# Performance work log

Measured on AMD Instinct MI355X. Metric: run time of the kernel, lower is better.

## Reference

```python
import jax, jax.numpy as jnp
import numpy as np
import math

B, H, S, DIM = 1, 16, 2048, 128

def _clin(xr, xi, wr, wi, br, bi):
    # complex linear: F.linear semantics -> x @ W.T
    out_r = xr @ wr.T - xi @ wi.T + br
    out_i = xr @ wi.T + xi @ wr.T + bi
    return out_r, out_i

def setup_inputs() -> dict:
    key = jax.random.key(0)
    ks = jax.random.split(key, 32)
    shp = (B, H, S, DIM)
    names = ["q_r", "q_i", "k_r", "k_i", "v_r", "v_i", "pe_q_r", "pe_q_i", "pe_k_r", "pe_k_i"]
    d = {n: jax.random.normal(ks[i], shp, jnp.float32) for i, n in enumerate(names)}
    wscale = 1.0 / math.sqrt(DIM)
    i = 10
    for p in ["q", "k", "v", "g", "o"]:
        d[p + "w_r"] = jax.random.normal(ks[i], (DIM, DIM), jnp.float32) * wscale; i += 1
        d[p + "w_i"] = jax.random.normal(ks[i], (DIM, DIM), jnp.float32) * wscale; i += 1
        d[p + "b_r"] = jnp.zeros((DIM,), jnp.float32)
        d[p + "b_i"] = jnp.zeros((DIM,), jnp.float32)
    return d

def reference(q_r, q_i, k_r, k_i, v_r, v_i, pe_q_r, pe_q_i, pe_k_r, pe_k_i,
              qw_r, qw_i, qb_r, qb_i, kw_r, kw_i, kb_r, kb_i,
              vw_r, vw_i, vb_r, vb_i, gw_r, gw_i, gb_r, gb_i,
              ow_r, ow_i, ob_r, ob_i):
    scale = DIM ** -0.5
    qr, qi = _clin(q_r, q_i, qw_r, qw_i, qb_r, qb_i)
    kr, ki = _clin(k_r, k_i, kw_r, kw_i, kb_r, kb_i)
    vr, vi = _clin(v_r, v_i, vw_r, vw_i, vb_r, vb_i)
    qr = qr + pe_q_r; qi = qi + pe_q_i
    kr = kr + pe_k_r; ki = ki + pe_k_i
    # complex QK^H -> real/imag parts, shapes [B,H,S,S]
    sr = jnp.einsum('bhqd,bhkd->bhqk', qr, kr) + jnp.einsum('bhqd,bhkd->bhqk', qi, ki)
    si = jnp.einsum('bhqd,bhkd->bhqk', qi, kr) - jnp.einsum('bhqd,bhkd->bhqk', qr, ki)
    scores = jnp.sqrt(sr * sr + si * si + 1e-8) * scale  # magnitude scores
    attn = jax.nn.softmax(scores, axis=-1)
    ar = attn @ vr
    ai = attn @ vi
    gr, gi = _clin(q_r, q_i, gw_r, gw_i, gb_r, gb_i)  # gate from raw q
    gar = gr * ar - gi * ai
    gai = gr * ai + gi * ar
    out_r, out_i = _clin(gar, gai, ow_r, ow_i, ob_r, ob_i)
    return (out_r, out_i, gr, gi)
```

## Files before the change

### kernel.cpp

```cpp
#include <hip/hip_runtime.h>
#include <math.h>

#define HH 16
#define SS 2048
#define DD 128
#define NROWS (HH * SS)
#define OUTSZ (HH * SS * DD)

typedef __attribute__((ext_vector_type(8))) short bf16x8;
typedef __attribute__((ext_vector_type(4))) float f32x4;
typedef __attribute__((ext_vector_type(8))) unsigned short u16x8;

#define MFMA16(a, b, c) __builtin_amdgcn_mfma_f32_16x16x32_bf16(a, b, c, 0, 0, 0)

__device__ __forceinline__ unsigned short f2bf(float f) {
    unsigned u = __float_as_uint(f);
    return (unsigned short)((u + 0x7FFFu + ((u >> 16) & 1u)) >> 16);
}
__device__ __forceinline__ bf16x8 negf(bf16x8 a) {
    bf16x8 r;
#pragma unroll
    for (int j = 0; j < 8; ++j) r[j] = (short)(a[j] ^ (short)0x8000);
    return r;
}

struct ClinPtrs {
    const float* xr; const float* xi;
    const float* gr; const float* gi;
    const float* wr; const float* wi;
    const float* br; const float* bi;
    const float* per; const float* pei;
    void* yr; void* yi;
    int outbf;
};

template <bool GATE>
__global__ __launch_bounds__(512, 2)
void clin_mfma(ClinPtrs P0, ClinPtrs P1, ClinPtrs P2, ClinPtrs P3) {
    __shared__ unsigned short wsh[2][DD][136];

    const int py = blockIdx.y;
    const ClinPtrs P = (py == 0) ? P0 : (py == 1) ? P1 : (py == 2) ? P2 : P3;

    const int t = threadIdx.x;
#pragma unroll
    for (int u = 0; u < 8; ++u) {
        const int f = t + 512 * u;
        const int c = f >> 11;
        const int rem = f & 2047;
        const int row = rem >> 4;
        const int g8 = (rem & 15) * 8;
        const float* src = (c ? P.wi : P.wr) + (long)row * DD + g8;
        const float4 a = *(const float4*)src;
        const float4 b = *(const float4*)(src + 4);
        unsigned short tmp[8] = {f2bf(a.x), f2bf(a.y), f2bf(a.z), f2bf(a.w),
                                 f2bf(b.x), f2bf(b.y), f2bf(b.z), f2bf(b.w)};
        *(u16x8*)&wsh[c][row][g8] = *(u16x8*)tmp;
    }

    const int w = t >> 6, lane = t & 63;
    const int lm = lane & 15, quad = lane >> 4;
    const long m0 = (long)blockIdx.x * 128 + w * 16;

    bf16x8 xrf[4], xif[4];
    {
        const long rbase = (m0 + lm) * DD;
#pragma unroll
        for (int dk = 0; dk < 4; ++dk) {
            const long o = rbase + dk * 32 + quad * 8;
            const float4 a0 = *(const float4*)(P.xr + o);
            const float4 a1 = *(const float4*)(P.xr + o + 4);
            const float4 b0 = *(const float4*)(P.xi + o);
            const float4 b1 = *(const float4*)(P.xi + o + 4);
            float fr[8] = {a0.x, a0.y, a0.z, a0.w, a1.x, a1.y, a1.z, a1.w};
            float fi[8] = {b0.x, b0.y, b0.z, b0.w, b1.x, b1.y, b1.z, b1.w};
            if (GATE) {
                const float4 c0v = *(const float4*)(P.gr + o);
                const float4 c1v = *(const float4*)(P.gr + o + 4);
                const float4 d0v = *(const float4*)(P.gi + o);
                const float4 d1v = *(const float4*)(P.gi + o + 4);
                const float ur[8] = {c0v.x, c0v.y, c0v.z, c0v.w, c1v.x, c1v.y, c1v.z, c1v.w};
                const float ui[8] = {d0v.x, d0v.y, d0v.z, d0v.w, d1v.x, d1v.y, d1v.z, d1v.w};
#pragma unroll
                for (int j = 0; j < 8; ++j) {
                    const float pr = fr[j] * ur[j] - fi[j] * ui[j];
                    const float pi = fr[j] * ui[j] + fi[j] * ur[j];
                    fr[j] = pr; fi[j] = pi;
                }
            }
#pragma unroll
            for (int j = 0; j < 8; ++j) {
                xrf[dk][j] = (short)f2bf(fr[j]);
                xif[dk][j] = (short)f2bf(fi[j]);
            }
        }
    }

    f32x4 Or[8], Oi[8];
    const f32x4 z = {0.f, 0.f, 0.f, 0.f};
#pragma unroll
    for (int nt = 0; nt < 8; ++nt) { Or[nt] = z; Oi[nt] = z; }

    __syncthreads();

#pragma unroll
    for (int dk = 0; dk < 4; ++dk) {
        const bf16x8 nxi = negf(xif[dk]);
        const int off = dk * 32 + quad * 8;
#pragma unroll
        for (int nt = 0; nt < 8; ++nt) {
            const bf16x8 wrf = *(bf16x8*)&wsh[0][nt * 16 + lm][off];
            const bf16x8 wif = *(bf16x8*)&wsh[1][nt * 16 + lm][off];
            Or[nt] = MFMA16(xrf[dk], wrf, Or[nt]);
            Or[nt] = MFMA16(nxi,     wif, Or[nt]);
            Oi[nt] = MFMA16(xrf[dk], wif, Oi[nt]);
            Oi[nt] = MFMA16(xif[dk], wrf, Oi[nt]);
        }
    }

#pragma unroll
    for (int nt = 0; nt < 8; ++nt) {
        const int c = nt * 16 + lm;
        const float bra = P.br[c], bia = P.bi[c];
#pragma unroll
        for (int reg = 0; reg < 4; ++reg) {
            const long R = m0 + quad * 4 + reg;
            float vr = Or[nt][reg] + bra;
            float vi = Oi[nt][reg] + bia;
            if (P.per != nullptr) {
                vr += P.per[R * DD + c];
                vi += P.pei[R * DD + c];
            }
            if (P.outbf) {
                ((unsigned short*)P.yr)[R * DD + c] = f2bf(vr);
                ((unsigned short*)P.yi)[R * DD + c] = f2bf(vi);
            } else {
                ((float*)P.yr)[R * DD + c] = vr;
                ((float*)P.yi)[R * DD + c] = vi;
            }
        }
    }
}

__global__ __launch_bounds__(512, 2)
void attn_mfma(const unsigned short* __restrict__ qr, const unsigned short* __restrict__ qi,
               const unsigned short* __restrict__ kr, const unsigned short* __restrict__ ki,
               const unsigned short* __restrict__ vr, const unsigned short* __restrict__ vi,
               float* __restrict__ out_r, float* __restrict__ out_i) {
    __shared__ unsigned short ks[2][2][32][136];
    __shared__ unsigned short vt[2][2][DD][40];
    __shared__ unsigned short ps[128][40];

    const int t = threadIdx.x;
    const int w = t >> 6, lane = t & 63;
    const int lm = lane & 15, quad = lane >> 4;

    const int bid = blockIdx.x;
    const int xcd = bid & 7;
    const int rr = bid >> 3;
    const int qt = rr & 15;
    const int h  = xcd + 8 * (rr >> 4);
    const long hbase = (long)h * SS * DD;
    const int q0 = qt * 128;
    const float scale = 0.08838834764831845f;

    int kC[2], kR[2], kG[2];
    const unsigned short* kp[2];
#pragma unroll
    for (int u = 0; u < 2; ++u) {
        const int f = t + 512 * u;
        kC[u] = f >> 9;
        kR[u] = (f & 511) >> 4;
        kG[u] = (f & 15) * 8;
        kp[u] = (kC[u] ? ki : kr) + hbase + (long)kR[u] * DD + kG[u];
    }
    const int vC = t >> 8;
    const int vS2 = (t & 15) * 2;
    const int vD8 = ((t >> 4) & 15) * 8;
    const unsigned short* vp = (vC ? vi : vr) + hbase + (long)vS2 * DD + vD8;

    u16x8 kA0, kA1, vA0, vA1;
    kA0 = *(const u16x8*)(kp[0]);
    kA1 = *(const u16x8*)(kp[1]);
    vA0 = *(const u16x8*)(vp);
    vA1 = *(const u16x8*)(vp + DD);

    bf16x8 qrf[4], qif[4];
    {
        const long rb = hbase + (long)(q0 + w * 16 + lm) * DD;
#pragma unroll
        for (int dk = 0; dk < 4; ++dk) {
            qrf[dk] = *(const bf16x8*)(qr + rb + dk * 32 + quad * 8);
            qif[dk] = *(const bf16x8*)(qi + rb + dk * 32 + quad * 8);
        }
    }

    f32x4 Or[8], Oi[8];
    const f32x4 z = {0.f, 0.f, 0.f, 0.f};
#pragma unroll
    for (int nt = 0; nt < 8; ++nt) { Or[nt] = z; Oi[nt] = z; }
    float l_st[4] = {0.f, 0.f, 0.f, 0.f};

#pragma unroll
    for (int u = 0; u < 2; ++u)
        *(u16x8*)&ks[0][kC[u]][kR[u]][kG[u]] = (u ? kA1 : kA0);
#pragma unroll
    for (int j = 0; j < 8; ++j) {
        const unsigned val = (unsigned)(unsigned short)vA0[j] |
                             ((unsigned)(unsigned short)vA1[j] << 16);
        *(unsigned*)&vt[0][vC][vD8 + j][vS2] = val;
    }
    __syncthreads();

    for (int kt = 0; kt < SS / 32; ++kt) {
        const int b = kt & 1;
        if (kt + 1 < SS / 32) {
            const long koff = (long)(kt + 1) * 32 * DD;
            kA0 = *(const u16x8*)(kp[0] + koff);
            kA1 = *(const u16x8*)(kp[1] + koff);
            vA0 = *(const u16x8*)(vp + koff);
            vA1 = *(const u16x8*)(vp + koff + DD);
        }

        f32x4 sr0 = z, sr1 = z, si0 = z, si1 = z;
#pragma unroll
        for (int dk = 0; dk < 4; ++dk) {
            const int off = dk * 32 + quad * 8;
            const bf16x8 kr0 = *(bf16x8*)&ks[b][0][lm][off];
            const bf16x8 ki0 = *(bf16x8*)&ks[b][1][lm][off];
            const bf16x8 kr1 = *(bf16x8*)&ks[b][0][16 + lm][off];
            const bf16x8 ki1 = *(bf16x8*)&ks[b][1][16 + lm][off];
            const bf16x8 nq = negf(qrf[dk]);
            sr0 = MFMA16(qrf[dk], kr0, sr0);  sr0 = MFMA16(qif[dk], ki0, sr0);
            si0 = MFMA16(qif[dk], kr0, si0);  si0 = MFMA16(nq, ki0, si0);
            sr1 = MFMA16(qrf[dk], kr1, sr1);  sr1 = MFMA16(qif[dk], ki1, sr1);
            si1 = MFMA16(qif[dk], kr1, si1);  si1 = MFMA16(nq, ki1, si1);
        }

#pragma unroll
        for (int reg = 0; reg < 4; ++reg) {
            const float s0 = __builtin_amdgcn_sqrtf(
                fmaf(sr0[reg], sr0[reg], fmaf(si0[reg], si0[reg], 1e-8f))) * scale;
            const float s1 = __builtin_amdgcn_sqrtf(
                fmaf(sr1[reg], sr1[reg], fmaf(si1[reg], si1[reg], 1e-8f))) * scale;
            const float p0 = __expf(s0);
            const float p1 = __expf(s1);
            l_st[reg] += p0 + p1;
            ps[w * 16 + quad * 4 + reg][lm]      = f2bf(p0);
            ps[w * 16 + quad * 4 + reg][16 + lm] = f2bf(p1);
        }

        const bf16x8 pf = *(bf16x8*)&ps[w * 16 + lm][quad * 8];
#pragma unroll
        for (int nt = 0; nt < 8; ++nt) {
            const bf16x8 vrf = *(bf16x8*)&vt[b][0][nt * 16 + lm][quad * 8];
            const bf16x8 vif = *(bf16x8*)&vt[b][1][nt * 16 + lm][quad * 8];
            Or[nt] = MFMA16(pf, vrf, Or[nt]);
            Oi[nt] = MFMA16(pf, vif, Oi[nt]);
        }

        if (kt + 1 < SS / 32) {
            __syncthreads();
#pragma unroll
            for (int u = 0; u < 2; ++u)
                *(u16x8*)&ks[b ^ 1][kC[u]][kR[u]][kG[u]] = (u ? kA1 : kA0);
#pragma unroll
            for (int j = 0; j < 8; ++j) {
                const unsigned val = (unsigned)(unsigned short)vA0[j] |
                                     ((unsigned)(unsigned short)vA1[j] << 16);
                *(unsigned*)&vt[b ^ 1][vC][vD8 + j][vS2] = val;
            }
            __syncthreads();
        }
    }

    float linv[4];
#pragma unroll
    for (int reg = 0; reg < 4; ++reg) {
        float l = l_st[reg];
#pragma unroll
        for (int off = 1; off < 16; off <<= 1) l += __shfl_xor(l, off);
        linv[reg] = 1.f / l;
    }
    const long ob = hbase + (long)(q0 + w * 16) * DD;
#pragma unroll
    for (int nt = 0; nt < 8; ++nt) {
        const int c = nt * 16 + lm;
#pragma unroll
        for (int reg = 0; reg < 4; ++reg) {
            const long R = ob + (long)(quad * 4 + reg) * DD + c;
            out_r[R] = Or[nt][reg] * linv[reg];
            out_i[R] = Oi[nt][reg] * linv[reg];
        }
    }
}

extern "C" void kernel_launch(void* const* d_in, const int* in_sizes, int n_in,
                              void* d_out, int out_size, void* d_ws, size_t ws_size,
                              hipStream_t stream) {
    const float* q_r    = (const float*)d_in[0];
    const float* q_i    = (const float*)d_in[1];
    const float* k_r    = (const float*)d_in[2];
    const float* k_i    = (const float*)d_in[3];
    const float* v_r    = (const float*)d_in[4];
    const float* v_i    = (const float*)d_in[5];
    const float* pe_q_r = (const float*)d_in[6];
    const float* pe_q_i = (const float*)d_in[7];
    const float* pe_k_r = (const float*)d_in[8];
    const float* pe_k_i = (const float*)d_in[9];
    const float* qw_r = (const float*)d_in[10];
    const float* qw_i = (const float*)d_in[11];
    const float* qb_r = (const float*)d_in[12];
    const float* qb_i = (const float*)d_in[13];
    const float* kw_r = (const float*)d_in[14];
    const float* kw_i = (const float*)d_in[15];
    const float* kb_r = (const float*)d_in[16];
    const float* kb_i = (const float*)d_in[17];
    const float* vw_r = (const float*)d_in[18];
    const float* vw_i = (const float*)d_in[19];
    const float* vb_r = (const float*)d_in[20];
    const float* vb_i = (const float*)d_in[21];
    const float* gw_r = (const float*)d_in[22];
    const float* gw_i = (const float*)d_in[23];
    const float* gb_r = (const float*)d_in[24];
    const float* gb_i = (const float*)d_in[25];
    const float* ow_r = (const float*)d_in[26];
    const float* ow_i = (const float*)d_in[27];
    const float* ob_r = (const float*)d_in[28];
    const float* ob_i = (const float*)d_in[29];

    float* out_r = (float*)d_out;
    float* out_i = out_r + (long)OUTSZ;
    float* g_r   = out_r + 2L * OUTSZ;
    float* g_i   = out_r + 3L * OUTSZ;

    unsigned short* ws = (unsigned short*)d_ws;
    unsigned short* pqr = ws + 0L * OUTSZ;
    unsigned short* pqi = ws + 1L * OUTSZ;
    unsigned short* pkr = ws + 2L * OUTSZ;
    unsigned short* pki = ws + 3L * OUTSZ;
    unsigned short* pvr = ws + 4L * OUTSZ;
    unsigned short* pvi = ws + 5L * OUTSZ;

    const dim3 blk(512);

    ClinPtrs P0 = {q_r, q_i, nullptr, nullptr, qw_r, qw_i, qb_r, qb_i,
                   pe_q_r, pe_q_i, pqr, pqi, 1};
    ClinPtrs P1 = {k_r, k_i, nullptr, nullptr, kw_r, kw_i, kb_r, kb_i,
                   pe_k_r, pe_k_i, pkr, pki, 1};
    ClinPtrs P2 = {v_r, v_i, nullptr, nullptr, vw_r, vw_i, vb_r, vb_i,
                   nullptr, nullptr, pvr, pvi, 1};
    ClinPtrs P3 = {q_r, q_i, nullptr, nullptr, gw_r, gw_i, gb_r, gb_i,
                   nullptr, nullptr, g_r, g_i, 0};

    clin_mfma<false><<<dim3(NROWS / 128, 4), blk, 0, stream>>>(P0, P1, P2, P3);

    attn_mfma<<<dim3((SS / 128) * HH), blk, 0, stream>>>(
        pqr, pqi, pkr, pki, pvr, pvi, out_r, out_i);

    ClinPtrs PF = {g_r, g_i, out_r, out_i, ow_r, ow_i, ob_r, ob_i,
                   nullptr, nullptr, out_r, out_i, 0};
    clin_mfma<true><<<dim3(NROWS / 128, 1), blk, 0, stream>>>(PF, PF, PF, PF);
}
```

Measured before the change: 428.4 us.

## Give each attention wave two 16-row query tiles with 256-thread blocks

The attention kernel now runs with 4 waves per block instead of 8, and each wave handles 32 query rows as two 16-row sub-tiles. Every K and V fragment read from shared memory is reused across both sub-tiles, which halves LDS reads per MFMA, and the negated Q fragments are computed once up front instead of on every iteration. In exchange each wave holds twice the accumulators and Q fragments, which raises register pressure (launch bounds now 256,1), and there are fewer waves per block to hide latency.

```diff
diff --git a/kernel.cpp b/kernel.cpp
--- a/kernel.cpp
+++ b/kernel.cpp
@@ -142,7 +142,7 @@
     }
 }
 
-__global__ __launch_bounds__(512, 2)
+__global__ __launch_bounds__(256, 1)
 void attn_mfma(const unsigned short* __restrict__ qr, const unsigned short* __restrict__ qi,
                const unsigned short* __restrict__ kr, const unsigned short* __restrict__ ki,
                const unsigned short* __restrict__ vr, const unsigned short* __restrict__ vi,
@@ -164,133 +164,166 @@
     const int q0 = qt * 128;
     const float scale = 0.08838834764831845f;
 
-    int kC[2], kR[2], kG[2];
-    const unsigned short* kp[2];
-#pragma unroll
-    for (int u = 0; u < 2; ++u) {
-        const int f = t + 512 * u;
+    int kC[4], kR[4], kG[4];
+    const unsigned short* kp[4];
+#pragma unroll
+    for (int u = 0; u < 4; ++u) {
+        const int f = t + 256 * u;
         kC[u] = f >> 9;
         kR[u] = (f & 511) >> 4;
         kG[u] = (f & 15) * 8;
         kp[u] = (kC[u] ? ki : kr) + hbase + (long)kR[u] * DD + kG[u];
     }
-    const int vC = t >> 8;
-    const int vS2 = (t & 15) * 2;
-    const int vD8 = ((t >> 4) & 15) * 8;
-    const unsigned short* vp = (vC ? vi : vr) + hbase + (long)vS2 * DD + vD8;
-
-    u16x8 kA0, kA1, vA0, vA1;
-    kA0 = *(const u16x8*)(kp[0]);
-    kA1 = *(const u16x8*)(kp[1]);
-    vA0 = *(const u16x8*)(vp);
-    vA1 = *(const u16x8*)(vp + DD);
-
-    bf16x8 qrf[4], qif[4];
-    {
-        const long rb = hbase + (long)(q0 + w * 16 + lm) * DD;
+    int vC[2], vS2[2], vD8[2];
+    const unsigned short* vp[2];
+#pragma unroll
+    for (int u = 0; u < 2; ++u) {
+        const int f = t + 256 * u;
+        vC[u] = f >> 8;
+        vS2[u] = (f & 15) * 2;
+        vD8[u] = ((f >> 4) & 15) * 8;
+        vp[u] = (vC[u] ? vi : vr) + hbase + (long)vS2[u] * DD + vD8[u];
+    }
+
+    u16x8 kA[4], vA0[2], vA1[2];
+#pragma unroll
+    for (int u = 0; u < 4; ++u) kA[u] = *(const u16x8*)(kp[u]);
+#pragma unroll
+    for (int u = 0; u < 2; ++u) {
+        vA0[u] = *(const u16x8*)(vp[u]);
+        vA1[u] = *(const u16x8*)(vp[u] + DD);
+    }
+
+    bf16x8 qrf[2][4], qif[2][4], nqrf[2][4];
+#pragma unroll
+    for (int s = 0; s < 2; ++s) {
+        const long rb = hbase + (long)(q0 + w * 32 + s * 16 + lm) * DD;
 #pragma unroll
         for (int dk = 0; dk < 4; ++dk) {
-            qrf[dk] = *(const bf16x8*)(qr + rb + dk * 32 + quad * 8);
-            qif[dk] = *(const bf16x8*)(qi + rb + dk * 32 + quad * 8);
-        }
-    }
-
-    f32x4 Or[8], Oi[8];
+            qrf[s][dk] = *(const bf16x8*)(qr + rb + dk * 32 + quad * 8);
+            qif[s][dk] = *(const bf16x8*)(qi + rb + dk * 32 + quad * 8);
+            nqrf[s][dk] = negf(qrf[s][dk]);
+        }
+    }
+
+    f32x4 Or[2][8], Oi[2][8];
     const f32x4 z = {0.f, 0.f, 0.f, 0.f};
 #pragma unroll
-    for (int nt = 0; nt < 8; ++nt) { Or[nt] = z; Oi[nt] = z; }
-    float l_st[4] = {0.f, 0.f, 0.f, 0.f};
-
+    for (int s = 0; s < 2; ++s)
+#pragma unroll
+        for (int nt = 0; nt < 8; ++nt) { Or[s][nt] = z; Oi[s][nt] = z; }
+    float l_st[2][4] = {{0.f, 0.f, 0.f, 0.f}, {0.f, 0.f, 0.f, 0.f}};
+
+#pragma unroll
+    for (int u = 0; u < 4; ++u)
+        *(u16x8*)&ks[0][kC[u]][kR[u]][kG[u]] = kA[u];
 #pragma unroll
     for (int u = 0; u < 2; ++u)
-        *(u16x8*)&ks[0][kC[u]][kR[u]][kG[u]] = (u ? kA1 : kA0);
-#pragma unroll
-    for (int j = 0; j < 8; ++j) {
-        const unsigned val = (unsigned)(unsigned short)vA0[j] |
-                             ((unsigned)(unsigned short)vA1[j] << 16);
-        *(unsigned*)&vt[0][vC][vD8 + j][vS2] = val;
-    }
+#pragma unroll
+        for (int j = 0; j < 8; ++j) {
+            const unsigned val = (unsigned)(unsigned short)vA0[u][j] |
+                                 ((unsigned)(unsigned short)vA1[u][j] << 16);
+            *(unsigned*)&vt[0][vC[u]][vD8[u] + j][vS2[u]] = val;
+        }
     __syncthreads();
 
     for (int kt = 0; kt < SS / 32; ++kt) {
         const int b = kt & 1;
         if (kt + 1 < SS / 32) {
             const long koff = (long)(kt + 1) * 32 * DD;
-            kA0 = *(const u16x8*)(kp[0] + koff);
-            kA1 = *(const u16x8*)(kp[1] + koff);
-            vA0 = *(const u16x8*)(vp + koff);
-            vA1 = *(const u16x8*)(vp + koff + DD);
-        }
-
-        f32x4 sr0 = z, sr1 = z, si0 = z, si1 = z;
+#pragma unroll
+            for (int u = 0; u < 4; ++u) kA[u] = *(const u16x8*)(kp[u] + koff);
+#pragma unroll
+            for (int u = 0; u < 2; ++u) {
+                vA0[u] = *(const u16x8*)(vp[u] + koff);
+                vA1[u] = *(const u16x8*)(vp[u] + koff + DD);
+            }
+        }
+
+        f32x4 sr0[2] = {z, z}, sr1[2] = {z, z}, si0[2] = {z, z}, si1[2] = {z, z};
 #pragma unroll
         for (int dk = 0; dk < 4; ++dk) {
             const int off = dk * 32 + quad * 8;
-            const bf16x8 kr0 = *(bf16x8*)&ks[b][0][lm][off];
-            const bf16x8 ki0 = *(bf16x8*)&ks[b][1][lm][off];
-            const bf16x8 kr1 = *(bf16x8*)&ks[b][0][16 + lm][off];
-            const bf16x8 ki1 = *(bf16x8*)&ks[b][1][16 + lm][off];
-            const bf16x8 nq = negf(qrf[dk]);
-            sr0 = MFMA16(qrf[dk], kr0, sr0);  sr0 = MFMA16(qif[dk], ki0, sr0);
-            si0 = MFMA16(qif[dk], kr0, si0);  si0 = MFMA16(nq, ki0, si0);
-            sr1 = MFMA16(qrf[dk], kr1, sr1);  sr1 = MFMA16(qif[dk], ki1, sr1);
-            si1 = MFMA16(qif[dk], kr1, si1);  si1 = MFMA16(nq, ki1, si1);
-        }
-
-#pragma unroll
-        for (int reg = 0; reg < 4; ++reg) {
-            const float s0 = __builtin_amdgcn_sqrtf(
-                fmaf(sr0[reg], sr0[reg], fmaf(si0[reg], si0[reg], 1e-8f))) * scale;
-            const float s1 = __builtin_amdgcn_sqrtf(
-                fmaf(sr1[reg], sr1[reg], fmaf(si1[reg], si1[reg], 1e-8f))) * scale;
-            const float p0 = __expf(s0);
-            const float p1 = __expf(s1);
-            l_st[reg] += p0 + p1;
-            ps[w * 16 + quad * 4 + reg][lm]      = f2bf(p0);
-            ps[w * 16 + quad * 4 + reg][16 + lm] = f2bf(p1);
-        }
-
-        const bf16x8 pf = *(bf16x8*)&ps[w * 16 + lm][quad * 8];
+            const bf16x8 kf0 = *(bf16x8*)&ks[b][0][lm][off];
+            const bf16x8 kg0 = *(bf16x8*)&ks[b][1][lm][off];
+            const bf16x8 kf1 = *(bf16x8*)&ks[b][0][16 + lm][off];
+            const bf16x8 kg1 = *(bf16x8*)&ks[b][1][16 + lm][off];
+#pragma unroll
+            for (int s = 0; s < 2; ++s) {
+                sr0[s] = MFMA16(qrf[s][dk], kf0, sr0[s]);  sr0[s] = MFMA16(qif[s][dk], kg0, sr0[s]);
+                si0[s] = MFMA16(qif[s][dk], kf0, si0[s]);  si0[s] = MFMA16(nqrf[s][dk], kg0, si0[s]);
+                sr1[s] = MFMA16(qrf[s][dk], kf1, sr1[s]);  sr1[s] = MFMA16(qif[s][dk], kg1, sr1[s]);
+                si1[s] = MFMA16(qif[s][dk], kf1, si1[s]);  si1[s] = MFMA16(nqrf[s][dk], kg1, si1[s]);
+            }
+        }
+
+#pragma unroll
+        for (int s = 0; s < 2; ++s)
+#pragma unroll
+            for (int reg = 0; reg < 4; ++reg) {
+                const float s0 = __builtin_amdgcn_sqrtf(
+                    fmaf(sr0[s][reg], sr0[s][reg], fmaf(si0[s][reg], si0[s][reg], 1e-8f))) * scale;
+                const float s1 = __builtin_amdgcn_sqrtf(
+                    fmaf(sr1[s][reg], sr1[s][reg], fmaf(si1[s][reg], si1[s][reg], 1e-8f))) * scale;
+                const float p0 = __expf(s0);
+                const float p1 = __expf(s1);
+                l_st[s][reg] += p0 + p1;
+                ps[w * 32 + s * 16 + quad * 4 + reg][lm]      = f2bf(p0);
+                ps[w * 32 + s * 16 + quad * 4 + reg][16 + lm] = f2bf(p1);
+            }
+
+        bf16x8 pf[2];
+#pragma unroll
+        for (int s = 0; s < 2; ++s)
+            pf[s] = *(bf16x8*)&ps[w * 32 + s * 16 + lm][quad * 8];
 #pragma unroll
         for (int nt = 0; nt < 8; ++nt) {
             const bf16x8 vrf = *(bf16x8*)&vt[b][0][nt * 16 + lm][quad * 8];
             const bf16x8 vif = *(bf16x8*)&vt[b][1][nt * 16 + lm][quad * 8];
-            Or[nt] = MFMA16(pf, vrf, Or[nt]);
-            Oi[nt] = MFMA16(pf, vif, Oi[nt]);
+#pragma unroll
+            for (int s = 0; s < 2; ++s) {
+                Or[s][nt] = MFMA16(pf[s], vrf, Or[s][nt]);
+                Oi[s][nt] = MFMA16(pf[s], vif, Oi[s][nt]);
+            }
         }
 
         if (kt + 1 < SS / 32) {
             __syncthreads();
 #pragma unroll
+            for (int u = 0; u < 4; ++u)
+                *(u16x8*)&ks[b ^ 1][kC[u]][kR[u]][kG[u]] = kA[u];
+#pragma unroll
             for (int u = 0; u < 2; ++u)
-                *(u16x8*)&ks[b ^ 1][kC[u]][kR[u]][kG[u]] = (u ? kA1 : kA0);
-#pragma unroll
-            for (int j = 0; j < 8; ++j) {
-                const unsigned val = (unsigned)(unsigned short)vA0[j] |
-                                     ((unsigned)(unsigned short)vA1[j] << 16);
-                *(unsigned*)&vt[b ^ 1][vC][vD8 + j][vS2] = val;
-            }
+#pragma unroll
+                for (int j = 0; j < 8; ++j) {
+                    const unsigned val = (unsigned)(unsigned short)vA0[u][j] |
+                                         ((unsigned)(unsigned short)vA1[u][j] << 16);
+                    *(unsigned*)&vt[b ^ 1][vC[u]][vD8[u] + j][vS2[u]] = val;
+                }
             __syncthreads();
         }
     }
 
-    float linv[4];
-#pragma unroll
-    for (int reg = 0; reg < 4; ++reg) {
-        float l = l_st[reg];
-#pragma unroll
-        for (int off = 1; off < 16; off <<= 1) l += __shfl_xor(l, off);
-        linv[reg] = 1.f / l;
-    }
-    const long ob = hbase + (long)(q0 + w * 16) * DD;
-#pragma unroll
-    for (int nt = 0; nt < 8; ++nt) {
-        const int c = nt * 16 + lm;
+#pragma unroll
+    for (int s = 0; s < 2; ++s) {
+        float linv[4];
 #pragma unroll
         for (int reg = 0; reg < 4; ++reg) {
-            const long R = ob + (long)(quad * 4 + reg) * DD + c;
-            out_r[R] = Or[nt][reg] * linv[reg];
-            out_i[R] = Oi[nt][reg] * linv[reg];
+            float l = l_st[s][reg];
+#pragma unroll
+            for (int off = 1; off < 16; off <<= 1) l += __shfl_xor(l, off);
+            linv[reg] = 1.f / l;
+        }
+        const long ob = hbase + (long)(q0 + w * 32 + s * 16) * DD;
+#pragma unroll
+        for (int nt = 0; nt < 8; ++nt) {
+            const int c = nt * 16 + lm;
+#pragma unroll
+            for (int reg = 0; reg < 4; ++reg) {
+                const long R = ob + (long)(quad * 4 + reg) * DD + c;
+                out_r[R] = Or[s][nt][reg] * linv[reg];
+                out_i[R] = Oi[s][nt][reg] * linv[reg];
+            }
         }
     }
 }
@@ -355,7 +388,7 @@
 
     clin_mfma<false><<<dim3(NROWS / 128, 4), blk, 0, stream>>>(P0, P1, P2, P3);
 
-    attn_mfma<<<dim3((SS / 128) * HH), blk, 0, stream>>>(
+    attn_mfma<<<dim3((SS / 128) * HH), dim3(256), 0, stream>>>(
         pqr, pqi, pkr, pki, pvr, pvi, out_r, out_i);
 
     ClinPtrs PF = {g_r, g_i, out_r, out_i, ow_r, ow_i, ob_r, ob_i,
```

After: 440.6 us. 1.03x slower.

## Stream multiple row tiles per block in projection kernel with register prefetch

Applied to the files above, without the earlier changes.

The projection kernel now has each block process four 128-row tiles instead of one, so the bf16 weight conversion into shared memory happens once per 512 rows. The next tile's activations are prefetched into registers while the current tile runs through the MFMAs, overlapping global loads with compute. The grid shrinks to 64x4 blocks. The gated output projection is split into its own specialized kernel. Risks are higher register pressure from two raw tile buffers and fewer blocks to fill the GPU.

```diff
diff --git a/kernel.cpp b/kernel.cpp
--- a/kernel.cpp
+++ b/kernel.cpp
@@ -26,7 +26,6 @@
 
 struct ClinPtrs {
     const float* xr; const float* xi;
-    const float* gr; const float* gi;
     const float* wr; const float* wi;
     const float* br; const float* bi;
     const float* per; const float* pei;
@@ -34,15 +33,49 @@
     int outbf;
 };
 
-template <bool GATE>
+struct RawA { float4 v[16]; };
+
+__device__ __forceinline__ void load_tile(RawA& r, const float* xr, const float* xi,
+                                          long rbase, int quad) {
+#pragma unroll
+    for (int dk = 0; dk < 4; ++dk) {
+        const long o = rbase + dk * 32 + quad * 8;
+        r.v[dk * 4 + 0] = *(const float4*)(xr + o);
+        r.v[dk * 4 + 1] = *(const float4*)(xr + o + 4);
+        r.v[dk * 4 + 2] = *(const float4*)(xi + o);
+        r.v[dk * 4 + 3] = *(const float4*)(xi + o + 4);
+    }
+}
+__device__ __forceinline__ void conv_tile(const RawA& r, bf16x8* xrf, bf16x8* xif) {
+#pragma unroll
+    for (int dk = 0; dk < 4; ++dk) {
+        const float4 a0 = r.v[dk * 4 + 0], a1 = r.v[dk * 4 + 1];
+        const float4 b0 = r.v[dk * 4 + 2], b1 = r.v[dk * 4 + 3];
+        const float fr[8] = {a0.x, a0.y, a0.z, a0.w, a1.x, a1.y, a1.z, a1.w};
+        const float fi[8] = {b0.x, b0.y, b0.z, b0.w, b1.x, b1.y, b1.z, b1.w};
+#pragma unroll
+        for (int j = 0; j < 8; ++j) {
+            xrf[dk][j] = (short)f2bf(fr[j]);
+            xif[dk][j] = (short)f2bf(fi[j]);
+        }
+    }
+}
+
 __global__ __launch_bounds__(512, 2)
-void clin_mfma(ClinPtrs P0, ClinPtrs P1, ClinPtrs P2, ClinPtrs P3) {
+void clin_stream(ClinPtrs P0, ClinPtrs P1, ClinPtrs P2, ClinPtrs P3) {
     __shared__ unsigned short wsh[2][DD][136];
 
     const int py = blockIdx.y;
     const ClinPtrs P = (py == 0) ? P0 : (py == 1) ? P1 : (py == 2) ? P2 : P3;
 
     const int t = threadIdx.x;
+    const int w = t >> 6, lane = t & 63;
+    const int lm = lane & 15, quad = lane >> 4;
+    const long blockRow0 = (long)blockIdx.x * 512;
+
+    RawA rawA, rawB;
+    load_tile(rawA, P.xr, P.xi, (blockRow0 + w * 16 + lm) * DD, quad);
+
 #pragma unroll
     for (int u = 0; u < 8; ++u) {
         const int f = t + 512 * u;
@@ -57,6 +90,89 @@
                                  f2bf(b.x), f2bf(b.y), f2bf(b.z), f2bf(b.w)};
         *(u16x8*)&wsh[c][row][g8] = *(u16x8*)tmp;
     }
+    __syncthreads();
+
+    const f32x4 z = {0.f, 0.f, 0.f, 0.f};
+
+#pragma unroll
+    for (int tt = 0; tt < 4; ++tt) {
+        RawA& cur = (tt & 1) ? rawB : rawA;
+        RawA& nxt = (tt & 1) ? rawA : rawB;
+        if (tt < 3)
+            load_tile(nxt, P.xr, P.xi,
+                      (blockRow0 + (tt + 1) * 128 + w * 16 + lm) * DD, quad);
+
+        bf16x8 xrf[4], xif[4];
+        conv_tile(cur, xrf, xif);
+
+        f32x4 Or[8], Oi[8];
+#pragma unroll
+        for (int nt = 0; nt < 8; ++nt) { Or[nt] = z; Oi[nt] = z; }
+
+#pragma unroll
+        for (int dk = 0; dk < 4; ++dk) {
+            const bf16x8 nxi = negf(xif[dk]);
+            const int off = dk * 32 + quad * 8;
+#pragma unroll
+            for (int nt = 0; nt < 8; ++nt) {
+                const bf16x8 wrf = *(bf16x8*)&wsh[0][nt * 16 + lm][off];
+                const bf16x8 wif = *(bf16x8*)&wsh[1][nt * 16 + lm][off];
+                Or[nt] = MFMA16(xrf[dk], wrf, Or[nt]);
+                Or[nt] = MFMA16(nxi,     wif, Or[nt]);
+                Oi[nt] = MFMA16(xrf[dk], wif, Oi[nt]);
+                Oi[nt] = MFMA16(xif[dk], wrf, Oi[nt]);
+            }
+        }
+
+        const long m0 = blockRow0 + tt * 128 + w * 16;
+#pragma unroll
+        for (int nt = 0; nt < 8; ++nt) {
+            const int c = nt * 16 + lm;
+            const float bra = P.br[c], bia = P.bi[c];
+#pragma unroll
+            for (int reg = 0; reg < 4; ++reg) {
+                const long R = m0 + quad * 4 + reg;
+                float vr = Or[nt][reg] + bra;
+                float vi = Oi[nt][reg] + bia;
+                if (P.per != nullptr) {
+                    vr += P.per[R * DD + c];
+                    vi += P.pei[R * DD + c];
+                }
+                if (P.outbf) {
+                    ((unsigned short*)P.yr)[R * DD + c] = f2bf(vr);
+                    ((unsigned short*)P.yi)[R * DD + c] = f2bf(vi);
+                } else {
+                    ((float*)P.yr)[R * DD + c] = vr;
+                    ((float*)P.yi)[R * DD + c] = vi;
+                }
+            }
+        }
+    }
+}
+
+__global__ __launch_bounds__(512, 2)
+void clin_gate(const float* __restrict__ xr, const float* __restrict__ xi,
+               const float* __restrict__ gr, const float* __restrict__ gi,
+               const float* __restrict__ wr, const float* __restrict__ wi,
+               const float* __restrict__ br, const float* __restrict__ bi,
+               float* __restrict__ yr, float* __restrict__ yi) {
+    __shared__ unsigned short wsh[2][DD][136];
+
+    const int t = threadIdx.x;
+#pragma unroll
+    for (int u = 0; u < 8; ++u) {
+        const int f = t + 512 * u;
+        const int c = f >> 11;
+        const int rem = f & 2047;
+        const int row = rem >> 4;
+        const int g8 = (rem & 15) * 8;
+        const float* src = (c ? wi : wr) + (long)row * DD + g8;
+        const float4 a = *(const float4*)src;
+        const float4 b = *(const float4*)(src + 4);
+        unsigned short tmp[8] = {f2bf(a.x), f2bf(a.y), f2bf(a.z), f2bf(a.w),
+                                 f2bf(b.x), f2bf(b.y), f2bf(b.z), f2bf(b.w)};
+        *(u16x8*)&wsh[c][row][g8] = *(u16x8*)tmp;
+    }
 
     const int w = t >> 6, lane = t & 63;
     const int lm = lane & 15, quad = lane >> 4;
@@ -68,30 +184,24 @@
 #pragma unroll
         for (int dk = 0; dk < 4; ++dk) {
             const long o = rbase + dk * 32 + quad * 8;
-            const float4 a0 = *(const float4*)(P.xr + o);
-            const float4 a1 = *(const float4*)(P.xr + o + 4);
-            const float4 b0 = *(const float4*)(P.xi + o);
-            const float4 b1 = *(const float4*)(P.xi + o + 4);
-            float fr[8] = {a0.x, a0.y, a0.z, a0.w, a1.x, a1.y, a1.z, a1.w};
-            float fi[8] = {b0.x, b0.y, b0.z, b0.w, b1.x, b1.y, b1.z, b1.w};
-            if (GATE) {
-                const float4 c0v = *(const float4*)(P.gr + o);
-                const float4 c1v = *(const float4*)(P.gr + o + 4);
-                const float4 d0v = *(const float4*)(P.gi + o);
-                const float4 d1v = *(const float4*)(P.gi + o + 4);
-                const float ur[8] = {c0v.x, c0v.y, c0v.z, c0v.w, c1v.x, c1v.y, c1v.z, c1v.w};
-                const float ui[8] = {d0v.x, d0v.y, d0v.z, d0v.w, d1v.x, d1v.y, d1v.z, d1v.w};
-#pragma unroll
-                for (int j = 0; j < 8; ++j) {
-                    const float pr = fr[j] * ur[j] - fi[j] * ui[j];
-                    const float pi = fr[j] * ui[j] + fi[j] * ur[j];
-                    fr[j] = pr; fi[j] = pi;
-                }
-            }
+            const float4 a0 = *(const float4*)(xr + o);
+            const float4 a1 = *(const float4*)(xr + o + 4);
+            const float4 b0 = *(const float4*)(xi + o);
+            const float4 b1 = *(const float4*)(xi + o + 4);
+            const float4 c0v = *(const float4*)(gr + o);
+            const float4 c1v = *(const float4*)(gr + o + 4);
+            const float4 d0v = *(const float4*)(gi + o);
+            const float4 d1v = *(const float4*)(gi + o + 4);
+            const float fr[8] = {a0.x, a0.y, a0.z, a0.w, a1.x, a1.y, a1.z, a1.w};
+            const float fi[8] = {b0.x, b0.y, b0.z, b0.w, b1.x, b1.y, b1.z, b1.w};
+            const float ur[8] = {c0v.x, c0v.y, c0v.z, c0v.w, c1v.x, c1v.y, c1v.z, c1v.w};
+            const float ui[8] = {d0v.x, d0v.y, d0v.z, d0v.w, d1v.x, d1v.y, d1v.z, d1v.w};
 #pragma unroll
             for (int j = 0; j < 8; ++j) {
-                xrf[dk][j] = (short)f2bf(fr[j]);
-                xif[dk][j] = (short)f2bf(fi[j]);
+                const float pr = fr[j] * ur[j] - fi[j] * ui[j];
+                const float pi = fr[j] * ui[j] + fi[j] * ur[j];
+                xrf[dk][j] = (short)f2bf(pr);
+                xif[dk][j] = (short)f2bf(pi);
             }
         }
     }
@@ -121,23 +231,12 @@
 #pragma unroll
     for (int nt = 0; nt < 8; ++nt) {
         const int c = nt * 16 + lm;
-        const float bra = P.br[c], bia = P.bi[c];
+        const float bra = br[c], bia = bi[c];
 #pragma unroll
         for (int reg = 0; reg < 4; ++reg) {
             const long R = m0 + quad * 4 + reg;
-            float vr = Or[nt][reg] + bra;
-            float vi = Oi[nt][reg] + bia;
-            if (P.per != nullptr) {
-                vr += P.per[R * DD + c];
-                vi += P.pei[R * DD + c];
-            }
-            if (P.outbf) {
-                ((unsigned short*)P.yr)[R * DD + c] = f2bf(vr);
-                ((unsigned short*)P.yi)[R * DD + c] = f2bf(vi);
-            } else {
-                ((float*)P.yr)[R * DD + c] = vr;
-                ((float*)P.yi)[R * DD + c] = vi;
-            }
+            yr[R * DD + c] = Or[nt][reg] + bra;
+            yi[R * DD + c] = Oi[nt][reg] + bia;
         }
     }
 }
@@ -344,21 +443,16 @@
 
     const dim3 blk(512);
 
-    ClinPtrs P0 = {q_r, q_i, nullptr, nullptr, qw_r, qw_i, qb_r, qb_i,
-                   pe_q_r, pe_q_i, pqr, pqi, 1};
-    ClinPtrs P1 = {k_r, k_i, nullptr, nullptr, kw_r, kw_i, kb_r, kb_i,
-                   pe_k_r, pe_k_i, pkr, pki, 1};
-    ClinPtrs P2 = {v_r, v_i, nullptr, nullptr, vw_r, vw_i, vb_r, vb_i,
-                   nullptr, nullptr, pvr, pvi, 1};
-    ClinPtrs P3 = {q_r, q_i, nullptr, nullptr, gw_r, gw_i, gb_r, gb_i,
-                   nullptr, nullptr, g_r, g_i, 0};
-
-    clin_mfma<false><<<dim3(NROWS / 128, 4), blk, 0, stream>>>(P0, P1, P2, P3);
+    ClinPtrs P0 = {q_r, q_i, qw_r, qw_i, qb_r, qb_i, pe_q_r, pe_q_i, pqr, pqi, 1};
+    ClinPtrs P1 = {k_r, k_i, kw_r, kw_i, kb_r, kb_i, pe_k_r, pe_k_i, pkr, pki, 1};
+    ClinPtrs P2 = {v_r, v_i, vw_r, vw_i, vb_r, vb_i, nullptr, nullptr, pvr, pvi, 1};
+    ClinPtrs P3 = {q_r, q_i, gw_r, gw_i, gb_r, gb_i, nullptr, nullptr, g_r, g_i, 0};
+
+    clin_stream<<<dim3(64, 4), blk, 0, stream>>>(P0, P1, P2, P3);
 
     attn_mfma<<<dim3((SS / 128) * HH), blk, 0, stream>>>(
         pqr, pqi, pkr, pki, pvr, pvi, out_r, out_i);
 
-    ClinPtrs PF = {g_r, g_i, out_r, out_i, ow_r, ow_i, ob_r, ob_i,
-                   nullptr, nullptr, out_r, out_i, 0};
-    clin_mfma<true><<<dim3(NROWS / 128, 1), blk, 0, stream>>>(PF, PF, PF, PF);
-}
+    clin_gate<<<dim3(NROWS / 128), blk, 0, stream>>>(
+        g_r, g_i, out_r, out_i, ow_r, ow_i, ob_r, ob_i, out_r, out_i);
+}
```

Result: slower. 457.7 us (+6.9%).

## Split complex linear by output-column halves with multi-tile rows and prefetch

Applied to the files above, without the earlier changes.

The complex linear kernel now computes only 64 output columns per block, split across a z grid dimension. This halves the shared weight tile so more blocks can be resident (launch bounds raised to 4). The projection pass loops over 4 row tiles per block, software-prefetching the next input chunk from registers, so each staged weight half is reused across rows. Attention output now goes to a separate workspace buffer so the final kernel's in-place read/write race on out_r/out_i disappears, at the cost of extra workspace and each input row being read twice, once per column half.

```diff
diff --git a/kernel.cpp b/kernel.cpp
--- a/kernel.cpp
+++ b/kernel.cpp
@@ -34,109 +34,140 @@
     int outbf;
 };
 
-template <bool GATE>
-__global__ __launch_bounds__(512, 2)
-void clin_mfma(ClinPtrs P0, ClinPtrs P1, ClinPtrs P2, ClinPtrs P3) {
-    __shared__ unsigned short wsh[2][DD][136];
+template <int TILES, bool GATE>
+__global__ __launch_bounds__(512, 4)
+void clin_half(ClinPtrs P0, ClinPtrs P1, ClinPtrs P2, ClinPtrs P3) {
+    __shared__ unsigned short wsh[2][64][136];
 
     const int py = blockIdx.y;
     const ClinPtrs P = (py == 0) ? P0 : (py == 1) ? P1 : (py == 2) ? P2 : P3;
 
+    const float* __restrict__ xr = P.xr;
+    const float* __restrict__ xi = P.xi;
+    const float* __restrict__ gr = P.gr;
+    const float* __restrict__ gi = P.gi;
+    const float* __restrict__ wr = P.wr;
+    const float* __restrict__ wi = P.wi;
+    const float* __restrict__ br = P.br;
+    const float* __restrict__ bi = P.bi;
+    const float* __restrict__ per = P.per;
+    const float* __restrict__ pei = P.pei;
+
     const int t = threadIdx.x;
-#pragma unroll
-    for (int u = 0; u < 8; ++u) {
+    const int w = t >> 6, lane = t & 63;
+    const int lm = lane & 15, quad = lane >> 4;
+    const int cb = blockIdx.z * 64;
+    const long rowA = (long)blockIdx.x * (128 * TILES);
+    const long tbase = rowA * DD + (long)(w * 16 + lm) * DD + quad * 8;
+
+    float4 raw[2][4];
+    {
+        const long o = tbase;
+        raw[0][0] = *(const float4*)(xr + o);
+        raw[0][1] = *(const float4*)(xr + o + 4);
+        raw[0][2] = *(const float4*)(xi + o);
+        raw[0][3] = *(const float4*)(xi + o + 4);
+    }
+
+#pragma unroll
+    for (int u = 0; u < 4; ++u) {
         const int f = t + 512 * u;
-        const int c = f >> 11;
-        const int rem = f & 2047;
+        const int c = f >> 10;
+        const int rem = f & 1023;
         const int row = rem >> 4;
         const int g8 = (rem & 15) * 8;
-        const float* src = (c ? P.wi : P.wr) + (long)row * DD + g8;
+        const float* src = (c ? wi : wr) + (long)(cb + row) * DD + g8;
         const float4 a = *(const float4*)src;
         const float4 b = *(const float4*)(src + 4);
         unsigned short tmp[8] = {f2bf(a.x), f2bf(a.y), f2bf(a.z), f2bf(a.w),
                                  f2bf(b.x), f2bf(b.y), f2bf(b.z), f2bf(b.w)};
         *(u16x8*)&wsh[c][row][g8] = *(u16x8*)tmp;
     }
-
-    const int w = t >> 6, lane = t & 63;
-    const int lm = lane & 15, quad = lane >> 4;
-    const long m0 = (long)blockIdx.x * 128 + w * 16;
-
-    bf16x8 xrf[4], xif[4];
-    {
-        const long rbase = (m0 + lm) * DD;
+    __syncthreads();
+
+    const f32x4 z = {0.f, 0.f, 0.f, 0.f};
+
+#pragma unroll
+    for (int tt = 0; tt < TILES; ++tt) {
+        f32x4 Or[4], Oi[4];
+#pragma unroll
+        for (int nt = 0; nt < 4; ++nt) { Or[nt] = z; Oi[nt] = z; }
+
 #pragma unroll
         for (int dk = 0; dk < 4; ++dk) {
-            const long o = rbase + dk * 32 + quad * 8;
-            const float4 a0 = *(const float4*)(P.xr + o);
-            const float4 a1 = *(const float4*)(P.xr + o + 4);
-            const float4 b0 = *(const float4*)(P.xi + o);
-            const float4 b1 = *(const float4*)(P.xi + o + 4);
-            float fr[8] = {a0.x, a0.y, a0.z, a0.w, a1.x, a1.y, a1.z, a1.w};
-            float fi[8] = {b0.x, b0.y, b0.z, b0.w, b1.x, b1.y, b1.z, b1.w};
-            if (GATE) {
-                const float4 c0v = *(const float4*)(P.gr + o);
-                const float4 c1v = *(const float4*)(P.gr + o + 4);
-                const float4 d0v = *(const float4*)(P.gi + o);
-                const float4 d1v = *(const float4*)(P.gi + o + 4);
-                const float ur[8] = {c0v.x, c0v.y, c0v.z, c0v.w, c1v.x, c1v.y, c1v.z, c1v.w};
-                const float ui[8] = {d0v.x, d0v.y, d0v.z, d0v.w, d1v.x, d1v.y, d1v.z, d1v.w};
+            const int step = tt * 4 + dk;
+            const int p = step & 1;
+            if (step + 1 < TILES * 4) {
+                const int ns = step + 1;
+                const long o = tbase + (long)(ns >> 2) * 128 * DD + (ns & 3) * 32;
+                raw[p ^ 1][0] = *(const float4*)(xr + o);
+                raw[p ^ 1][1] = *(const float4*)(xr + o + 4);
+                raw[p ^ 1][2] = *(const float4*)(xi + o);
+                raw[p ^ 1][3] = *(const float4*)(xi + o + 4);
+            }
+            bf16x8 xrf, xif;
+            {
+                const float4 a0 = raw[p][0], a1 = raw[p][1];
+                const float4 b0 = raw[p][2], b1 = raw[p][3];
+                float fr[8] = {a0.x, a0.y, a0.z, a0.w, a1.x, a1.y, a1.z, a1.w};
+                float fi[8] = {b0.x, b0.y, b0.z, b0.w, b1.x, b1.y, b1.z, b1.w};
+                if (GATE) {
+                    const long o = tbase + (long)tt * 128 * DD + dk * 32;
+                    const float4 c0v = *(const float4*)(gr + o);
+                    const float4 c1v = *(const float4*)(gr + o + 4);
+                    const float4 d0v = *(const float4*)(gi + o);
+                    const float4 d1v = *(const float4*)(gi + o + 4);
+                    const float ur[8] = {c0v.x, c0v.y, c0v.z, c0v.w,
+                                         c1v.x, c1v.y, c1v.z, c1v.w};
+                    const float ui[8] = {d0v.x, d0v.y, d0v.z, d0v.w,
+                                         d1v.x, d1v.y, d1v.z, d1v.w};
+#pragma unroll
+                    for (int j = 0; j < 8; ++j) {
+                        const float pr = fr[j] * ur[j] - fi[j] * ui[j];
+                        const float pi = fr[j] * ui[j] + fi[j] * ur[j];
+                        fr[j] = pr; fi[j] = pi;
+                    }
+                }
 #pragma unroll
                 for (int j = 0; j < 8; ++j) {
-                    const float pr = fr[j] * ur[j] - fi[j] * ui[j];
-                    const float pi = fr[j] * ui[j] + fi[j] * ur[j];
-                    fr[j] = pr; fi[j] = pi;
+                    xrf[j] = (short)f2bf(fr[j]);
+                    xif[j] = (short)f2bf(fi[j]);
                 }
             }
-#pragma unroll
-            for (int j = 0; j < 8; ++j) {
-                xrf[dk][j] = (short)f2bf(fr[j]);
-                xif[dk][j] = (short)f2bf(fi[j]);
-            }
-        }
-    }
-
-    f32x4 Or[8], Oi[8];
-    const f32x4 z = {0.f, 0.f, 0.f, 0.f};
-#pragma unroll
-    for (int nt = 0; nt < 8; ++nt) { Or[nt] = z; Oi[nt] = z; }
-
-    __syncthreads();
-
-#pragma unroll
-    for (int dk = 0; dk < 4; ++dk) {
-        const bf16x8 nxi = negf(xif[dk]);
-        const int off = dk * 32 + quad * 8;
-#pragma unroll
-        for (int nt = 0; nt < 8; ++nt) {
-            const bf16x8 wrf = *(bf16x8*)&wsh[0][nt * 16 + lm][off];
-            const bf16x8 wif = *(bf16x8*)&wsh[1][nt * 16 + lm][off];
-            Or[nt] = MFMA16(xrf[dk], wrf, Or[nt]);
-            Or[nt] = MFMA16(nxi,     wif, Or[nt]);
-            Oi[nt] = MFMA16(xrf[dk], wif, Oi[nt]);
-            Oi[nt] = MFMA16(xif[dk], wrf, Oi[nt]);
-        }
-    }
-
-#pragma unroll
-    for (int nt = 0; nt < 8; ++nt) {
-        const int c = nt * 16 + lm;
-        const float bra = P.br[c], bia = P.bi[c];
-#pragma unroll
-        for (int reg = 0; reg < 4; ++reg) {
-            const long R = m0 + quad * 4 + reg;
-            float vr = Or[nt][reg] + bra;
-            float vi = Oi[nt][reg] + bia;
-            if (P.per != nullptr) {
-                vr += P.per[R * DD + c];
-                vi += P.pei[R * DD + c];
-            }
-            if (P.outbf) {
-                ((unsigned short*)P.yr)[R * DD + c] = f2bf(vr);
-                ((unsigned short*)P.yi)[R * DD + c] = f2bf(vi);
-            } else {
-                ((float*)P.yr)[R * DD + c] = vr;
-                ((float*)P.yi)[R * DD + c] = vi;
+            const bf16x8 nxi = negf(xif);
+            const int off = dk * 32 + quad * 8;
+#pragma unroll
+            for (int nt = 0; nt < 4; ++nt) {
+                const bf16x8 wrf = *(bf16x8*)&wsh[0][nt * 16 + lm][off];
+                const bf16x8 wif = *(bf16x8*)&wsh[1][nt * 16 + lm][off];
+                Or[nt] = MFMA16(xrf, wrf, Or[nt]);
+                Or[nt] = MFMA16(nxi, wif, Or[nt]);
+                Oi[nt] = MFMA16(xrf, wif, Oi[nt]);
+                Oi[nt] = MFMA16(xif, wrf, Oi[nt]);
+            }
+        }
+
+        const long m0 = rowA + tt * 128 + w * 16;
+#pragma unroll
+        for (int nt = 0; nt < 4; ++nt) {
+            const int c = cb + nt * 16 + lm;
+            const float bra = br[c], bia = bi[c];
+#pragma unroll
+            for (int reg = 0; reg < 4; ++reg) {
+                const long R = m0 + quad * 4 + reg;
+                float vr = Or[nt][reg] + bra;
+                float vi = Oi[nt][reg] + bia;
+                if (per != nullptr) {
+                    vr += per[R * DD + c];
+                    vi += pei[R * DD + c];
+                }
+                if (P.outbf) {
+                    ((unsigned short*)P.yr)[R * DD + c] = f2bf(vr);
+                    ((unsigned short*)P.yi)[R * DD + c] = f2bf(vi);
+                } else {
+                    ((float*)P.yr)[R * DD + c] = vr;
+                    ((float*)P.yi)[R * DD + c] = vi;
+                }
             }
         }
     }
@@ -341,6 +372,8 @@
     unsigned short* pki = ws + 3L * OUTSZ;
     unsigned short* pvr = ws + 4L * OUTSZ;
     unsigned short* pvi = ws + 5L * OUTSZ;
+    float* aw_r = (float*)(ws + 6L * OUTSZ);
+    float* aw_i = aw_r + (long)OUTSZ;
 
     const dim3 blk(512);
 
@@ -353,12 +386,12 @@
     ClinPtrs P3 = {q_r, q_i, nullptr, nullptr, gw_r, gw_i, gb_r, gb_i,
                    nullptr, nullptr, g_r, g_i, 0};
 
-    clin_mfma<false><<<dim3(NROWS / 128, 4), blk, 0, stream>>>(P0, P1, P2, P3);
+    clin_half<4, false><<<dim3(64, 4, 2), blk, 0, stream>>>(P0, P1, P2, P3);
 
     attn_mfma<<<dim3((SS / 128) * HH), blk, 0, stream>>>(
-        pqr, pqi, pkr, pki, pvr, pvi, out_r, out_i);
-
-    ClinPtrs PF = {g_r, g_i, out_r, out_i, ow_r, ow_i, ob_r, ob_i,
+        pqr, pqi, pkr, pki, pvr, pvi, aw_r, aw_i);
+
+    ClinPtrs PF = {aw_r, aw_i, g_r, g_i, ow_r, ow_i, ob_r, ob_i,
                    nullptr, nullptr, out_r, out_i, 0};
-    clin_mfma<true><<<dim3(NROWS / 128, 1), blk, 0, stream>>>(PF, PF, PF, PF);
-}
+    clin_half<1, true><<<dim3(256, 1, 2), blk, 0, stream>>>(PF, PF, PF, PF);
+}
```

After: 449.6 us. +5.0%, slower.
